# Optimization experiments

Hardware: AMD Instinct MI355X
Metric: run time of the kernel (lower is better)

Reference implementation:

```python
import jax, jax.numpy as jnp
import numpy as np

H = 1024
NUM_HEADS = 16
HEAD_DIM = H // NUM_HEADS
EPS = 1e-6
GEN_E, GEN_IE = 8, 4096 // 8     # general experts, per-expert intermediate
MOD_E, MOD_IE = 4, 4096 // 4     # per-modality experts, per-expert intermediate


def layernorm(x, g, b):
    m = jnp.mean(x, axis=-1, keepdims=True)
    v = jnp.mean((x - m) ** 2, axis=-1, keepdims=True)
    return (x - m) * jax.lax.rsqrt(v + EPS) * g + b


def attention(x, qkv_w, qkv_b, proj_w, proj_b):
    B, N, _ = x.shape
    qkv = (x @ qkv_w + qkv_b).reshape(B, N, 3, NUM_HEADS, HEAD_DIM)
    qkv = jnp.transpose(qkv, (2, 0, 3, 1, 4))  # [3,B,h,N,d]
    q, k, v = qkv[0], qkv[1], qkv[2]
    scale = HEAD_DIM ** -0.5
    attn = jax.nn.softmax(jnp.einsum('bhnd,bhmd->bhnm', q, k) * scale, axis=-1)
    out = jnp.einsum('bhnm,bhmd->bhnd', attn, v)
    out = jnp.transpose(out, (0, 2, 1, 3)).reshape(B, N, H)
    return out @ proj_w + proj_b


def routed_mlp(x, position_ids, gate_up, down, ie):
    # expert_id = position % num_experts; compute all experts then select per token
    # (avoids materializing per-token [T,H,2I] gathered weights).
    E = gate_up.shape[0]
    eids = position_ids % E  # [B,N]
    gu = jnp.einsum('bnh,ehi->bnei', x, gate_up)              # [B,N,E,2*ie]
    gu = jnp.take_along_axis(gu, eids[..., None, None], axis=2)[:, :, 0]
    gate, up = gu[..., :ie], gu[..., ie:]
    inter = jax.nn.silu(gate) * up                             # [B,N,ie]
    dn = jnp.einsum('bni,eih->bneh', inter, down)              # [B,N,E,H]
    return jnp.take_along_axis(dn, eids[..., None, None], axis=2)[:, :, 0]


def setup_inputs() -> dict:
    key = jax.random.key(0)
    ks = jax.random.split(key, 16)
    B, N = 2, 2048
    inp = {
        'x': jax.random.normal(ks[0], (B, N, H), jnp.float32),
        'qkv_w': jax.random.normal(ks[1], (H, 3 * H), jnp.float32) * 0.02,
        'qkv_b': jnp.zeros((3 * H,), jnp.float32),
        'proj_w': jax.random.normal(ks[2], (H, H), jnp.float32) * 0.02,
        'proj_b': jnp.zeros((H,), jnp.float32),
        'ln1_g': jnp.ones((H,), jnp.float32), 'ln1_b': jnp.zeros((H,), jnp.float32),
        'ln2_g': jnp.ones((H,), jnp.float32), 'ln2_b': jnp.zeros((H,), jnp.float32),
        'ln3_g': jnp.ones((H,), jnp.float32), 'ln3_b': jnp.zeros((H,), jnp.float32),
        'gen_gu': jax.random.normal(ks[3], (GEN_E, H, 2 * GEN_IE), jnp.float32) * 0.02,
        'gen_dn': jax.random.normal(ks[4], (GEN_E, GEN_IE, H), jnp.float32) * 0.02,
        'text_gu': jax.random.normal(ks[5], (MOD_E, H, 2 * MOD_IE), jnp.float32) * 0.02,
        'text_dn': jax.random.normal(ks[6], (MOD_E, MOD_IE, H), jnp.float32) * 0.02,
        'img_gu': jax.random.normal(ks[7], (MOD_E, H, 2 * MOD_IE), jnp.float32) * 0.02,
        'img_dn': jax.random.normal(ks[8], (MOD_E, MOD_IE, H), jnp.float32) * 0.02,
        'aud_gu': jax.random.normal(ks[9], (MOD_E, H, 2 * MOD_IE), jnp.float32) * 0.02,
        'aud_dn': jax.random.normal(ks[10], (MOD_E, MOD_IE, H), jnp.float32) * 0.02,
        'vid_gu': jax.random.normal(ks[11], (MOD_E, H, 2 * MOD_IE), jnp.float32) * 0.02,
        'vid_dn': jax.random.normal(ks[12], (MOD_E, MOD_IE, H), jnp.float32) * 0.02,
        'modality_ids': jax.random.randint(ks[13], (B, N), 0, 4, jnp.int32),
        'position_ids': jnp.arange(B * N, dtype=jnp.int32).reshape(B, N),
    }
    return inp


def reference(x, qkv_w, qkv_b, proj_w, proj_b,
              ln1_g, ln1_b, ln2_g, ln2_b, ln3_g, ln3_b,
              gen_gu, gen_dn, text_gu, text_dn, img_gu, img_dn,
              aud_gu, aud_dn, vid_gu, vid_dn,
              modality_ids, position_ids):
    x = x + attention(layernorm(x, ln1_g, ln1_b), qkv_w, qkv_b, proj_w, proj_b)
    x = x + routed_mlp(layernorm(x, ln2_g, ln2_b), position_ids, gen_gu, gen_dn, GEN_IE)
    normed = layernorm(x, ln3_g, ln3_b)
    tm = (modality_ids == 0)[..., None].astype(x.dtype)
    im = (modality_ids == 1)[..., None].astype(x.dtype)
    am = (modality_ids == 2)[..., None].astype(x.dtype)
    vm = (modality_ids == 3)[..., None].astype(x.dtype)
    x = x + (routed_mlp(normed, position_ids, text_gu, text_dn, MOD_IE) * tm
             + routed_mlp(normed, position_ids, img_gu, img_dn, MOD_IE) * im
             + routed_mlp(normed, position_ids, aud_gu, aud_dn, MOD_IE) * am
             + routed_mlp(normed, position_ids, vid_gu, vid_dn, MOD_IE) * vm)
    return x
```

## Files before the change

### kernel.cpp

```cpp
#include <hip/hip_runtime.h>

#define T_TOKENS 4096
#define HDIM 1024

typedef __attribute__((ext_vector_type(8))) short bf16x8;
typedef __attribute__((ext_vector_type(4))) float f32x4;

static __device__ inline unsigned short f2bf(float f) {
  unsigned u = __float_as_uint(f);
  unsigned r = (u + 0x7FFFu + ((u >> 16) & 1u)) >> 16;
  return (unsigned short)r;
}
static __device__ inline float bf2f(unsigned short h) {
  unsigned u = ((unsigned)h) << 16;
  return __uint_as_float(u);
}
static __device__ __forceinline__ void gl16(const void* g, void* l) {
  __builtin_amdgcn_global_load_lds((const __attribute__((address_space(1))) void*)g,
                                   (__attribute__((address_space(3))) void*)l, 16, 0, 0);
}

__launch_bounds__(256)
__global__ void ln_kernel(const float* __restrict__ in, const float* __restrict__ g,
                          const float* __restrict__ b, unsigned short* __restrict__ out) {
  const int row = blockIdx.x;
  const int tid = threadIdx.x;
  const long base = (long)row * HDIM;
  float4 v = *(const float4*)(in + base + tid * 4);
  __shared__ float red[256];
  red[tid] = v.x + v.y + v.z + v.w;
  __syncthreads();
  for (int st = 128; st > 0; st >>= 1) {
    if (tid < st) red[tid] += red[tid + st];
    __syncthreads();
  }
  const float mean = red[0] * (1.f / HDIM);
  __syncthreads();
  const float dx = v.x - mean, dy = v.y - mean, dz = v.z - mean, dw = v.w - mean;
  red[tid] = dx * dx + dy * dy + dz * dz + dw * dw;
  __syncthreads();
  for (int st = 128; st > 0; st >>= 1) {
    if (tid < st) red[tid] += red[tid + st];
    __syncthreads();
  }
  const float rstd = rsqrtf(red[0] * (1.f / HDIM) + 1e-6f);
  const int c = tid * 4;
  const float4 g4 = *(const float4*)(g + c);
  const float4 b4 = *(const float4*)(b + c);
  uint2 o;
  o.x = (unsigned)f2bf(dx * rstd * g4.x + b4.x) | ((unsigned)f2bf(dy * rstd * g4.y + b4.y) << 16);
  o.y = (unsigned)f2bf(dz * rstd * g4.z + b4.z) | ((unsigned)f2bf(dw * rstd * g4.w + b4.w) << 16);
  *(uint2*)(out + base + c) = o;
}

__launch_bounds__(256)
__global__ void build_groups(const int* __restrict__ pids, const int* __restrict__ mids,
                             int* __restrict__ gen_cnt, int* __restrict__ gen_list,
                             int* __restrict__ mod_cnt, int* __restrict__ mod_list) {
  const int t = blockIdx.x * 256 + threadIdx.x;
  if (t >= T_TOKENS) return;
  const int p = pids[t];
  const int ge = p & 7;
  int s = atomicAdd(&gen_cnt[ge], 1);
  if (s < 512) gen_list[ge * 512 + s] = t;
  const int g = mids[t] * 4 + (p & 3);
  s = atomicAdd(&mod_cnt[g], 1);
  if (s < 1024) mod_list[g * 1024 + s] = t;
}

__launch_bounds__(256)
__global__ void convert_w(const float* __restrict__ W, unsigned short* __restrict__ Wt,
                          int K, int N) {
  const long zo = (long)blockIdx.z * K * N;
  const float* Wp = W + zo;
  unsigned short* Wo = Wt + zo;
  const int n0 = blockIdx.x * 64, k0 = blockIdx.y * 64;
  __shared__ float T[64][65];
  const int tid = threadIdx.x;
#pragma unroll
  for (int i = 0; i < 4; ++i) {
    const int item = tid + i * 256;
    const int kk = item >> 4, c4 = (item & 15) * 4;
    const float4 v = *(const float4*)(Wp + (long)(k0 + kk) * N + n0 + c4);
    T[c4 + 0][kk] = v.x; T[c4 + 1][kk] = v.y; T[c4 + 2][kk] = v.z; T[c4 + 3][kk] = v.w;
  }
  __syncthreads();
#pragma unroll
  for (int i = 0; i < 4; ++i) {
    const int item = tid + i * 256;
    const int nn = item >> 4, k4 = (item & 15) * 4;
    uint2 p;
    p.x = (unsigned)f2bf(T[nn][k4 + 0]) | ((unsigned)f2bf(T[nn][k4 + 1]) << 16);
    p.y = (unsigned)f2bf(T[nn][k4 + 2]) | ((unsigned)f2bf(T[nn][k4 + 3]) << 16);
    *(uint2*)(Wo + (long)(n0 + nn) * K + k0 + k4) = p;
  }
}

enum { MODE_DENSE = 0, MODE_GEN = 1, MODE_MOD = 2 };
enum { OM_F32R = 0, OM_BF16 = 1, OM_QKV = 2 };

template <int MODE, int OMODE, bool WBF16, bool BIAS>
__launch_bounds__(256)
__global__ void mgemm(const unsigned short* __restrict__ A,
                      const void* __restrict__ w0, const float* __restrict__ w1,
                      const float* __restrict__ w2, const float* __restrict__ w3,
                      long wstep, const float* __restrict__ bias,
                      const float* __restrict__ resid, void* __restrict__ Cout,
                      unsigned short* __restrict__ qb, unsigned short* __restrict__ kb,
                      unsigned short* __restrict__ vtb,
                      int K, int N,
                      const int* __restrict__ cnts, const int* __restrict__ rowlist,
                      int cap) {
  const int z = blockIdx.z;
  const int n0 = blockIdx.x * 128;
  const int m0 = blockIdx.y * 128;

  int Meff = 1 << 30;
  const int* list = nullptr;
  if constexpr (MODE != MODE_DENSE) {
    Meff = cnts[z];
    if (m0 >= Meff) return;
    list = rowlist + z * cap;
  }

  __shared__ char As[128 * 64 * 2];
  __shared__ char Bs[128 * 64 * 2];

  const int tid = threadIdx.x;
  const int w = tid >> 6;
  const int lane = tid & 63;
  const int wm = w >> 1, wn = w & 1;
  const int srow = lane >> 3, sc = lane & 7;

  const unsigned short* asrc[4];
  char* aldsb = As + w * 4096;
#pragma unroll
  for (int i = 0; i < 4; ++i) {
    const int r = w * 32 + i * 8 + srow;
    long tok;
    if constexpr (MODE == MODE_DENSE) {
      tok = m0 + r;
    } else {
      int gm = m0 + r;
      if (gm >= Meff) gm = Meff - 1;
      tok = (long)list[gm];
    }
    asrc[i] = A + tok * (long)K + (sc ^ (r & 7)) * 8;
  }

  const unsigned short* bsrc[4];
  char* bldsb = Bs + w * 4096;
  const float* bptr[4];
  int boff[4];
  if constexpr (WBF16) {
    const unsigned short* W = (const unsigned short*)w0;
    if constexpr (MODE != MODE_DENSE) W += (long)z * wstep;
#pragma unroll
    for (int i = 0; i < 4; ++i) {
      const int r = w * 32 + i * 8 + srow;
      bsrc[i] = W + (long)(n0 + r) * K + (sc ^ (r & 7)) * 8;
    }
  } else {
    const float* W;
    if constexpr (MODE == MODE_MOD) {
      const int mm = z >> 2;
      const float* basep = (mm == 0) ? (const float*)w0 : (mm == 1) ? w1 : (mm == 2) ? w2 : w3;
      W = basep + (long)(z & 3) * wstep;
    } else {
      W = (const float*)w0 + (MODE != MODE_DENSE ? (long)z * wstep : 0);
    }
#pragma unroll
    for (int j = 0; j < 4; ++j) {
      const int item = tid + j * 256;
      const int kc = item >> 7;
      const int nl = item & 127;
      bptr[j] = W + (long)(kc * 8) * N + n0 + nl;
      boff[j] = (nl * 128 + kc * 16) ^ ((nl & 7) << 4);
    }
  }

  f32x4 acc[4][4] = {};

  for (int kt = 0; kt < K; kt += 64) {
    __syncthreads();
#pragma unroll
    for (int i = 0; i < 4; ++i) gl16(asrc[i] + kt, aldsb + i * 1024);
    if constexpr (WBF16) {
#pragma unroll
      for (int i = 0; i < 4; ++i) gl16(bsrc[i] + kt, bldsb + i * 1024);
    } else {
#pragma unroll
      for (int j = 0; j < 4; ++j) {
        const float* bp = bptr[j] + (long)kt * N;
        float kv[8];
#pragma unroll
        for (int u = 0; u < 8; ++u) kv[u] = bp[(long)u * N];
        uint4 p;
        p.x = (unsigned)f2bf(kv[0]) | ((unsigned)f2bf(kv[1]) << 16);
        p.y = (unsigned)f2bf(kv[2]) | ((unsigned)f2bf(kv[3]) << 16);
        p.z = (unsigned)f2bf(kv[4]) | ((unsigned)f2bf(kv[5]) << 16);
        p.w = (unsigned)f2bf(kv[6]) | ((unsigned)f2bf(kv[7]) << 16);
        *(uint4*)(Bs + boff[j]) = p;
      }
    }
    __syncthreads();

#pragma unroll
    for (int kk = 0; kk < 2; ++kk) {
      const int kb2 = kk * 64 + (lane >> 4) * 16;
      bf16x8 af[4], bfr[4];
#pragma unroll
      for (int f = 0; f < 4; ++f) {
        const int ar = wm * 64 + f * 16 + (lane & 15);
        af[f] = *(bf16x8*)(As + ((ar * 128 + kb2) ^ ((ar & 7) << 4)));
        const int br = wn * 64 + f * 16 + (lane & 15);
        bfr[f] = *(bf16x8*)(Bs + ((br * 128 + kb2) ^ ((br & 7) << 4)));
      }
#pragma unroll
      for (int mf = 0; mf < 4; ++mf)
#pragma unroll
        for (int nf = 0; nf < 4; ++nf)
          acc[mf][nf] =
              __builtin_amdgcn_mfma_f32_16x16x32_bf16(af[mf], bfr[nf], acc[mf][nf], 0, 0, 0);
    }
  }

  const int lr4 = (lane >> 4) * 4;
  const int lc = lane & 15;
#pragma unroll
  for (int mf = 0; mf < 4; ++mf) {
#pragma unroll
    for (int r = 0; r < 4; ++r) {
      const int gm = m0 + wm * 64 + mf * 16 + lr4 + r;
      long orow;
      if constexpr (MODE == MODE_DENSE) {
        orow = gm;
      } else {
        if (gm >= Meff) continue;
        orow = (long)list[gm];
      }
#pragma unroll
      for (int nf = 0; nf < 4; ++nf) {
        const int gc = n0 + wn * 64 + nf * 16 + lc;
        float val = acc[mf][nf][r];
        if constexpr (BIAS) val += bias[gc];
        if constexpr (OMODE == OM_F32R) {
          val += resid[orow * (long)N + gc];
          ((float*)Cout)[orow * (long)N + gc] = val;
        } else if constexpr (OMODE == OM_BF16) {
          ((unsigned short*)Cout)[orow * (long)N + gc] = f2bf(val);
        } else {
          const int bb = (int)(orow >> 11), tl = (int)orow & 2047;
          const int seg = gc >> 10, hc = gc & 1023, h = hc >> 6, d = hc & 63;
          if (seg == 0)
            qb[(((long)(bb * 16 + h) * 2048) + tl) * 64 + d] = f2bf(val * 0.125f);
          else if (seg == 1)
            kb[(((long)(bb * 16 + h) * 2048) + tl) * 64 + d] = f2bf(val);
          else
            vtb[((long)(bb * 16 + h) * 64 + d) * 2048 + tl] = f2bf(val);
        }
      }
    }
  }
}

__launch_bounds__(256)
__global__ void attn_kernel(const unsigned short* __restrict__ Qb,
                            const unsigned short* __restrict__ Kb,
                            const unsigned short* __restrict__ Vtb,
                            unsigned short* __restrict__ out) {
  const int qt = blockIdx.x;
  const int bh = blockIdx.y;
  const int b = bh >> 4, h = bh & 15;
  const int tid = threadIdx.x;
  const int w = tid >> 6;
  const int lane = tid & 63;
  const int srow = lane >> 3, sc = lane & 7;

  __shared__ char Ksb[8192];
  __shared__ char Vsb[8192];
  __shared__ char Psb[8192];
  char* Pwb = Psb + w * 2048;

  const unsigned short* Qh = Qb + ((long)(b * 16 + h) * 2048 + qt * 64) * 64;
  const unsigned short* Kh = Kb + (long)(b * 16 + h) * 2048 * 64;
  const unsigned short* Vh = Vtb + (long)(b * 16 + h) * 64 * 2048;

  bf16x8 qf[2];
  {
    const int qr = w * 16 + (lane & 15);
#pragma unroll
    for (int kst = 0; kst < 2; ++kst)
      qf[kst] = *(const bf16x8*)(Qh + qr * 64 + kst * 32 + (lane >> 4) * 8);
  }

  const unsigned short* ksrc[2];
  const unsigned short* vsrc[2];
  char* kld = Ksb + w * 2048;
  char* vld = Vsb + w * 2048;
#pragma unroll
  for (int i = 0; i < 2; ++i) {
    const int r = w * 16 + i * 8 + srow;
    ksrc[i] = Kh + (long)r * 64 + (sc ^ (r & 7)) * 8;
    vsrc[i] = Vh + (long)r * 2048 + (sc ^ (r & 7)) * 8;
  }

  float m_run[4] = {-1e30f, -1e30f, -1e30f, -1e30f};
  float l_run[4] = {0.f, 0.f, 0.f, 0.f};
  f32x4 acc[4] = {};

  for (int kt = 0; kt < 32; ++kt) {
    __syncthreads();
#pragma unroll
    for (int i = 0; i < 2; ++i) gl16(ksrc[i] + (long)kt * 64 * 64, kld + i * 1024);
#pragma unroll
    for (int i = 0; i < 2; ++i) gl16(vsrc[i] + kt * 64, vld + i * 1024);
    __syncthreads();

    f32x4 sf[4] = {};
    {
      const int cb = (lane >> 4) * 16;
#pragma unroll
      for (int f = 0; f < 4; ++f) {
        const int krow = f * 16 + (lane & 15);
        const int sw = (krow & 7) << 4;
        const bf16x8 k0 = *(bf16x8*)(Ksb + ((krow * 128 + cb) ^ sw));
        const bf16x8 k1 = *(bf16x8*)(Ksb + ((krow * 128 + 64 + cb) ^ sw));
        sf[f] = __builtin_amdgcn_mfma_f32_16x16x32_bf16(qf[0], k0, sf[f], 0, 0, 0);
        sf[f] = __builtin_amdgcn_mfma_f32_16x16x32_bf16(qf[1], k1, sf[f], 0, 0, 0);
      }
    }
    float al[4];
#pragma unroll
    for (int r = 0; r < 4; ++r) {
      float m0 = fmaxf(fmaxf(sf[0][r], sf[1][r]), fmaxf(sf[2][r], sf[3][r]));
      m0 = fmaxf(m0, __shfl_xor(m0, 1));
      m0 = fmaxf(m0, __shfl_xor(m0, 2));
      m0 = fmaxf(m0, __shfl_xor(m0, 4));
      m0 = fmaxf(m0, __shfl_xor(m0, 8));
      const float mn = fmaxf(m_run[r], m0);
      al[r] = __expf(m_run[r] - mn);
      m_run[r] = mn;
    }
#pragma unroll
    for (int f = 0; f < 4; ++f)
#pragma unroll
      for (int r = 0; r < 4; ++r) sf[f][r] = __expf(sf[f][r] - m_run[r]);
#pragma unroll
    for (int r = 0; r < 4; ++r) {
      float rs = sf[0][r] + sf[1][r] + sf[2][r] + sf[3][r];
      rs += __shfl_xor(rs, 1);
      rs += __shfl_xor(rs, 2);
      rs += __shfl_xor(rs, 4);
      rs += __shfl_xor(rs, 8);
      l_run[r] = l_run[r] * al[r] + rs;
    }
#pragma unroll
    for (int d = 0; d < 4; ++d)
#pragma unroll
      for (int r = 0; r < 4; ++r) acc[d][r] *= al[r];

#pragma unroll
    for (int f = 0; f < 4; ++f)
#pragma unroll
      for (int r = 0; r < 4; ++r) {
        const int prow = (lane >> 4) * 4 + r;
        const int off = (prow * 128 + (f * 16 + (lane & 15)) * 2) ^ ((prow & 7) << 4);
        *(short*)(Pwb + off) = (short)f2bf(sf[f][r]);
      }
    {
      const int cb = (lane >> 4) * 16;
      const int prow = lane & 15;
      const int psw = (prow & 7) << 4;
      const bf16x8 p0 = *(bf16x8*)(Pwb + ((prow * 128 + cb) ^ psw));
      const bf16x8 p1 = *(bf16x8*)(Pwb + ((prow * 128 + 64 + cb) ^ psw));
#pragma unroll
      for (int d = 0; d < 4; ++d) {
        const int vrow = d * 16 + (lane & 15);
        const int vsw = (vrow & 7) << 4;
        const bf16x8 v0 = *(bf16x8*)(Vsb + ((vrow * 128 + cb) ^ vsw));
        const bf16x8 v1 = *(bf16x8*)(Vsb + ((vrow * 128 + 64 + cb) ^ vsw));
        acc[d] = __builtin_amdgcn_mfma_f32_16x16x32_bf16(p0, v0, acc[d], 0, 0, 0);
        acc[d] = __builtin_amdgcn_mfma_f32_16x16x32_bf16(p1, v1, acc[d], 0, 0, 0);
      }
    }
  }

  float invl[4];
#pragma unroll
  for (int r = 0; r < 4; ++r) invl[r] = 1.f / l_run[r];
  unsigned short* op = out + (long)(b * 2048 + qt * 64 + w * 16) * 1024 + h * 64;
#pragma unroll
  for (int f = 0; f < 4; ++f)
#pragma unroll
    for (int r = 0; r < 4; ++r) {
      const int row = (lane >> 4) * 4 + r;
      op[(long)row * 1024 + f * 16 + (lane & 15)] = f2bf(acc[f][r] * invl[r]);
    }
}

__launch_bounds__(256)
__global__ void silu_bf(const unsigned short* __restrict__ gu, unsigned short* __restrict__ inter,
                        int IE2, int IE, int shift) {
  const int total = T_TOKENS << shift;
  for (int idx = blockIdx.x * 256 + threadIdx.x; idx < total; idx += gridDim.x * 256) {
    const int t = idx >> shift;
    const int r8 = (idx & ((1 << shift) - 1)) * 8;
    const unsigned short* gp = gu + (long)t * IE2 + r8;
    const uint4 gg = *(const uint4*)gp;
    const uint4 uu = *(const uint4*)(gp + IE);
    const unsigned gw[4] = {gg.x, gg.y, gg.z, gg.w};
    const unsigned uw[4] = {uu.x, uu.y, uu.z, uu.w};
    uint4 o;
    unsigned ow[4];
#pragma unroll
    for (int q = 0; q < 4; ++q) {
      const float g0 = __uint_as_float(gw[q] << 16);
      const float g1 = __uint_as_float(gw[q] & 0xffff0000u);
      const float u0 = __uint_as_float(uw[q] << 16);
      const float u1 = __uint_as_float(uw[q] & 0xffff0000u);
      const float r0 = g0 / (1.f + __expf(-g0)) * u0;
      const float r1 = g1 / (1.f + __expf(-g1)) * u1;
      ow[q] = (unsigned)f2bf(r0) | ((unsigned)f2bf(r1) << 16);
    }
    o.x = ow[0]; o.y = ow[1]; o.z = ow[2]; o.w = ow[3];
    *(uint4*)(inter + (long)t * IE + r8) = o;
  }
}

extern "C" void kernel_launch(void* const* d_in, const int* in_sizes, int n_in,
                              void* d_out, int out_size, void* d_ws, size_t ws_size,
                              hipStream_t stream) {
  const float* x       = (const float*)d_in[0];
  const float* qkv_w   = (const float*)d_in[1];
  const float* qkv_b   = (const float*)d_in[2];
  const float* proj_w  = (const float*)d_in[3];
  const float* proj_b  = (const float*)d_in[4];
  const float* ln1_g   = (const float*)d_in[5];
  const float* ln1_b   = (const float*)d_in[6];
  const float* ln2_g   = (const float*)d_in[7];
  const float* ln2_b   = (const float*)d_in[8];
  const float* ln3_g   = (const float*)d_in[9];
  const float* ln3_b   = (const float*)d_in[10];
  const float* gen_gu  = (const float*)d_in[11];
  const float* gen_dn  = (const float*)d_in[12];
  const float* text_gu = (const float*)d_in[13];
  const float* text_dn = (const float*)d_in[14];
  const float* img_gu  = (const float*)d_in[15];
  const float* img_dn  = (const float*)d_in[16];
  const float* aud_gu  = (const float*)d_in[17];
  const float* aud_dn  = (const float*)d_in[18];
  const float* vid_gu  = (const float*)d_in[19];
  const float* vid_dn  = (const float*)d_in[20];
  const int* mids      = (const int*)d_in[21];
  const int* pids      = (const int*)d_in[22];
  float* out = (float*)d_out;
  char* ws = (char*)d_ws;

  const unsigned long MB = 1ul << 20;
  unsigned short* lnb   = (unsigned short*)(ws);
  unsigned short* Qb    = (unsigned short*)(ws + 8 * MB);
  unsigned short* Kb    = (unsigned short*)(ws + 16 * MB);
  unsigned short* Vtb   = (unsigned short*)(ws + 24 * MB);
  unsigned short* attno = (unsigned short*)(ws + 32 * MB);
  unsigned short* wqkv  = (unsigned short*)(ws + 40 * MB);
  unsigned short* wproj = (unsigned short*)(ws + 46 * MB);
  unsigned short* wggu  = (unsigned short*)(ws + 48 * MB);
  unsigned short* wgdn  = (unsigned short*)(ws + 64 * MB);
  int* gen_cnt  = (int*)(ws + 72 * MB);
  int* mod_cnt  = gen_cnt + 8;
  int* gen_list = gen_cnt + 32;
  int* mod_list = gen_list + 8 * 512;
  unsigned short* guo    = Qb;
  unsigned short* intero = Vtb;

  hipMemsetAsync(gen_cnt, 0, (8 + 16) * sizeof(int), stream);
  build_groups<<<16, 256, 0, stream>>>(pids, mids, gen_cnt, gen_list, mod_cnt, mod_list);

  convert_w<<<dim3(48, 16, 1), 256, 0, stream>>>(qkv_w, wqkv, 1024, 3072);
  convert_w<<<dim3(16, 16, 1), 256, 0, stream>>>(proj_w, wproj, 1024, 1024);
  convert_w<<<dim3(16, 16, 8), 256, 0, stream>>>(gen_gu, wggu, 1024, 1024);
  convert_w<<<dim3(16, 8, 8), 256, 0, stream>>>(gen_dn, wgdn, 512, 1024);

  ln_kernel<<<4096, 256, 0, stream>>>(x, ln1_g, ln1_b, lnb);
  mgemm<MODE_DENSE, OM_QKV, true, true><<<dim3(24, 32, 1), 256, 0, stream>>>(
      lnb, wqkv, nullptr, nullptr, nullptr, 0L, qkv_b, nullptr, nullptr,
      Qb, Kb, Vtb, 1024, 3072, nullptr, nullptr, 0);
  attn_kernel<<<dim3(32, 32, 1), 256, 0, stream>>>(Qb, Kb, Vtb, attno);
  mgemm<MODE_DENSE, OM_F32R, true, true><<<dim3(8, 32, 1), 256, 0, stream>>>(
      attno, wproj, nullptr, nullptr, nullptr, 0L, proj_b, x, out,
      nullptr, nullptr, nullptr, 1024, 1024, nullptr, nullptr, 0);

  ln_kernel<<<4096, 256, 0, stream>>>(out, ln2_g, ln2_b, lnb);
  mgemm<MODE_GEN, OM_BF16, true, false><<<dim3(8, 4, 8), 256, 0, stream>>>(
      lnb, wggu, nullptr, nullptr, nullptr, (long)1024 * 1024, nullptr, nullptr, guo,
      nullptr, nullptr, nullptr, 1024, 1024, gen_cnt, gen_list, 512);
  silu_bf<<<1024, 256, 0, stream>>>(guo, intero, 1024, 512, 6);
  mgemm<MODE_GEN, OM_F32R, true, false><<<dim3(8, 4, 8), 256, 0, stream>>>(
      intero, wgdn, nullptr, nullptr, nullptr, (long)1024 * 512, nullptr, out, out,
      nullptr, nullptr, nullptr, 512, 1024, gen_cnt, gen_list, 512);

  ln_kernel<<<4096, 256, 0, stream>>>(out, ln3_g, ln3_b, lnb);
  mgemm<MODE_MOD, OM_BF16, false, false><<<dim3(16, 8, 16), 256, 0, stream>>>(
      lnb, text_gu, img_gu, aud_gu, vid_gu, (long)1024 * 2048, nullptr, nullptr, guo,
      nullptr, nullptr, nullptr, 1024, 2048, mod_cnt, mod_list, 1024);
  silu_bf<<<2048, 256, 0, stream>>>(guo, intero, 2048, 1024, 7);
  mgemm<MODE_MOD, OM_F32R, false, false><<<dim3(8, 8, 16), 256, 0, stream>>>(
      intero, text_dn, img_dn, aud_dn, vid_dn, (long)1024 * 1024, nullptr, out, out,
      nullptr, nullptr, nullptr, 1024, 1024, mod_cnt, mod_list, 1024);
}
```

Before: 460.2 us.

## Restructure attention to 128-key tiles with transposed scores and exp2 softmax

The attention kernel now processes 128 keys per iteration instead of 64 and computes S^T (K as the A operand), so each lane holds one query's scores and row max/sum need only two cross-lane shuffles. The log2(e) factor is folded into the Q scaling so exp2 can replace expf, and P is written to LDS packed as pairs. Separately, the manual bf16 rounding is replaced with the hardware v_cvt_pk_bf16_f32 instruction across the layernorm, weight-conversion, GEMM and SiLU kernels. The larger tile doubles LDS use per block, which can lower occupancy.

```diff
diff --git a/kernel.cpp b/kernel.cpp
--- a/kernel.cpp
+++ b/kernel.cpp
@@ -5,15 +5,18 @@
 
 typedef __attribute__((ext_vector_type(8))) short bf16x8;
 typedef __attribute__((ext_vector_type(4))) float f32x4;
+
+#define EXP2F(x) __builtin_amdgcn_exp2f(x)
 
 static __device__ inline unsigned short f2bf(float f) {
   unsigned u = __float_as_uint(f);
   unsigned r = (u + 0x7FFFu + ((u >> 16) & 1u)) >> 16;
   return (unsigned short)r;
 }
-static __device__ inline float bf2f(unsigned short h) {
-  unsigned u = ((unsigned)h) << 16;
-  return __uint_as_float(u);
+static __device__ __forceinline__ unsigned cvtpk(float lo, float hi) {
+  unsigned r;
+  asm("v_cvt_pk_bf16_f32 %0, %1, %2" : "=v"(r) : "v"(lo), "v"(hi));
+  return r;
 }
 static __device__ __forceinline__ void gl16(const void* g, void* l) {
   __builtin_amdgcn_global_load_lds((const __attribute__((address_space(1))) void*)g,
@@ -48,8 +51,8 @@
   const float4 g4 = *(const float4*)(g + c);
   const float4 b4 = *(const float4*)(b + c);
   uint2 o;
-  o.x = (unsigned)f2bf(dx * rstd * g4.x + b4.x) | ((unsigned)f2bf(dy * rstd * g4.y + b4.y) << 16);
-  o.y = (unsigned)f2bf(dz * rstd * g4.z + b4.z) | ((unsigned)f2bf(dw * rstd * g4.w + b4.w) << 16);
+  o.x = cvtpk(dx * rstd * g4.x + b4.x, dy * rstd * g4.y + b4.y);
+  o.y = cvtpk(dz * rstd * g4.z + b4.z, dw * rstd * g4.w + b4.w);
   *(uint2*)(out + base + c) = o;
 }
 
@@ -90,8 +93,8 @@
     const int item = tid + i * 256;
     const int nn = item >> 4, k4 = (item & 15) * 4;
     uint2 p;
-    p.x = (unsigned)f2bf(T[nn][k4 + 0]) | ((unsigned)f2bf(T[nn][k4 + 1]) << 16);
-    p.y = (unsigned)f2bf(T[nn][k4 + 2]) | ((unsigned)f2bf(T[nn][k4 + 3]) << 16);
+    p.x = cvtpk(T[nn][k4 + 0], T[nn][k4 + 1]);
+    p.y = cvtpk(T[nn][k4 + 2], T[nn][k4 + 3]);
     *(uint2*)(Wo + (long)(n0 + nn) * K + k0 + k4) = p;
   }
 }
@@ -196,10 +199,10 @@
 #pragma unroll
         for (int u = 0; u < 8; ++u) kv[u] = bp[(long)u * N];
         uint4 p;
-        p.x = (unsigned)f2bf(kv[0]) | ((unsigned)f2bf(kv[1]) << 16);
-        p.y = (unsigned)f2bf(kv[2]) | ((unsigned)f2bf(kv[3]) << 16);
-        p.z = (unsigned)f2bf(kv[4]) | ((unsigned)f2bf(kv[5]) << 16);
-        p.w = (unsigned)f2bf(kv[6]) | ((unsigned)f2bf(kv[7]) << 16);
+        p.x = cvtpk(kv[0], kv[1]);
+        p.y = cvtpk(kv[2], kv[3]);
+        p.z = cvtpk(kv[4], kv[5]);
+        p.w = cvtpk(kv[6], kv[7]);
         *(uint4*)(Bs + boff[j]) = p;
       }
     }
@@ -253,7 +256,7 @@
           const int bb = (int)(orow >> 11), tl = (int)orow & 2047;
           const int seg = gc >> 10, hc = gc & 1023, h = hc >> 6, d = hc & 63;
           if (seg == 0)
-            qb[(((long)(bb * 16 + h) * 2048) + tl) * 64 + d] = f2bf(val * 0.125f);
+            qb[(((long)(bb * 16 + h) * 2048) + tl) * 64 + d] = f2bf(val * 0.18033688011112042f);
           else if (seg == 1)
             kb[(((long)(bb * 16 + h) * 2048) + tl) * 64 + d] = f2bf(val);
           else
@@ -275,127 +278,121 @@
   const int tid = threadIdx.x;
   const int w = tid >> 6;
   const int lane = tid & 63;
-  const int srow = lane >> 3, sc = lane & 7;
-
-  __shared__ char Ksb[8192];
-  __shared__ char Vsb[8192];
-  __shared__ char Psb[8192];
-  char* Pwb = Psb + w * 2048;
+  const int g = lane >> 4;
+  const int q = lane & 15;
+
+  __shared__ char Ksb[128 * 128];
+  __shared__ char Vsb[64 * 256];
+  __shared__ char Psb[4 * 16 * 256];
+  char* Pwb = Psb + w * 4096;
 
   const unsigned short* Qh = Qb + ((long)(b * 16 + h) * 2048 + qt * 64) * 64;
   const unsigned short* Kh = Kb + (long)(b * 16 + h) * 2048 * 64;
   const unsigned short* Vh = Vtb + (long)(b * 16 + h) * 64 * 2048;
 
   bf16x8 qf[2];
-  {
-    const int qr = w * 16 + (lane & 15);
-#pragma unroll
-    for (int kst = 0; kst < 2; ++kst)
-      qf[kst] = *(const bf16x8*)(Qh + qr * 64 + kst * 32 + (lane >> 4) * 8);
-  }
-
-  const unsigned short* ksrc[2];
-  const unsigned short* vsrc[2];
-  char* kld = Ksb + w * 2048;
-  char* vld = Vsb + w * 2048;
-#pragma unroll
-  for (int i = 0; i < 2; ++i) {
-    const int r = w * 16 + i * 8 + srow;
-    ksrc[i] = Kh + (long)r * 64 + (sc ^ (r & 7)) * 8;
-    vsrc[i] = Vh + (long)r * 2048 + (sc ^ (r & 7)) * 8;
-  }
-
-  float m_run[4] = {-1e30f, -1e30f, -1e30f, -1e30f};
-  float l_run[4] = {0.f, 0.f, 0.f, 0.f};
+#pragma unroll
+  for (int kst = 0; kst < 2; ++kst)
+    qf[kst] = *(const bf16x8*)(Qh + (w * 16 + q) * 64 + kst * 32 + g * 8);
+
+  const unsigned short* ksrc[4];
+  const unsigned short* vsrc[4];
+  char* kld = Ksb + w * 4096;
+  char* vld = Vsb + w * 4096;
+#pragma unroll
+  for (int i = 0; i < 4; ++i) {
+    const int r = w * 32 + i * 8 + (lane >> 3);
+    ksrc[i] = Kh + (long)r * 64 + ((lane & 7) ^ (r & 7)) * 8;
+    const int d = w * 16 + i * 4 + (lane >> 4);
+    vsrc[i] = Vh + (long)d * 2048 + ((lane & 15) ^ (d & 7)) * 8;
+  }
+
+  float m_run = -1e30f, l_run = 0.f;
   f32x4 acc[4] = {};
-
-  for (int kt = 0; kt < 32; ++kt) {
+  const int qsw = (q & 7) << 4;
+
+  for (int kt = 0; kt < 16; ++kt) {
     __syncthreads();
 #pragma unroll
-    for (int i = 0; i < 2; ++i) gl16(ksrc[i] + (long)kt * 64 * 64, kld + i * 1024);
-#pragma unroll
-    for (int i = 0; i < 2; ++i) gl16(vsrc[i] + kt * 64, vld + i * 1024);
+    for (int i = 0; i < 4; ++i) gl16(ksrc[i] + (long)kt * 128 * 64, kld + i * 1024);
+#pragma unroll
+    for (int i = 0; i < 4; ++i) gl16(vsrc[i] + kt * 128, vld + i * 1024);
     __syncthreads();
 
-    f32x4 sf[4] = {};
-    {
-      const int cb = (lane >> 4) * 16;
-#pragma unroll
-      for (int f = 0; f < 4; ++f) {
-        const int krow = f * 16 + (lane & 15);
-        const int sw = (krow & 7) << 4;
-        const bf16x8 k0 = *(bf16x8*)(Ksb + ((krow * 128 + cb) ^ sw));
-        const bf16x8 k1 = *(bf16x8*)(Ksb + ((krow * 128 + 64 + cb) ^ sw));
-        sf[f] = __builtin_amdgcn_mfma_f32_16x16x32_bf16(qf[0], k0, sf[f], 0, 0, 0);
-        sf[f] = __builtin_amdgcn_mfma_f32_16x16x32_bf16(qf[1], k1, sf[f], 0, 0, 0);
+    f32x4 sf[8];
+#pragma unroll
+    for (int f = 0; f < 8; ++f) {
+      const int krow = f * 16 + q;
+      const int sw = (krow & 7) << 4;
+      const bf16x8 k0 = *(bf16x8*)(Ksb + krow * 128 + ((g * 16) ^ sw));
+      const bf16x8 k1 = *(bf16x8*)(Ksb + krow * 128 + ((64 + g * 16) ^ sw));
+      f32x4 t = {};
+      t = __builtin_amdgcn_mfma_f32_16x16x32_bf16(k0, qf[0], t, 0, 0, 0);
+      sf[f] = __builtin_amdgcn_mfma_f32_16x16x32_bf16(k1, qf[1], t, 0, 0, 0);
+    }
+
+    float mx = sf[0][0];
+#pragma unroll
+    for (int f = 0; f < 8; ++f) {
+      mx = fmaxf(mx, fmaxf(fmaxf(sf[f][0], sf[f][1]), fmaxf(sf[f][2], sf[f][3])));
+    }
+    mx = fmaxf(mx, __shfl_xor(mx, 16));
+    mx = fmaxf(mx, __shfl_xor(mx, 32));
+    const float mn = fmaxf(m_run, mx);
+    const float alpha = EXP2F(m_run - mn);
+    m_run = mn;
+
+    float ls = 0.f;
+#pragma unroll
+    for (int f = 0; f < 8; ++f) {
+#pragma unroll
+      for (int r = 0; r < 4; ++r) {
+        sf[f][r] = EXP2F(sf[f][r] - mn);
       }
-    }
-    float al[4];
+      ls += (sf[f][0] + sf[f][1]) + (sf[f][2] + sf[f][3]);
+    }
+    ls += __shfl_xor(ls, 16);
+    ls += __shfl_xor(ls, 32);
+    l_run = l_run * alpha + ls;
+
+#pragma unroll
+    for (int f = 0; f < 8; ++f) {
+      const unsigned p0 = cvtpk(sf[f][0], sf[f][1]);
+      const unsigned p1 = cvtpk(sf[f][2], sf[f][3]);
+      const int base = f * 32 + g * 8;
+      *(unsigned*)(Pwb + q * 256 + ((base) ^ qsw)) = p0;
+      *(unsigned*)(Pwb + q * 256 + ((base + 4) ^ qsw)) = p1;
+    }
+
 #pragma unroll
     for (int r = 0; r < 4; ++r) {
-      float m0 = fmaxf(fmaxf(sf[0][r], sf[1][r]), fmaxf(sf[2][r], sf[3][r]));
-      m0 = fmaxf(m0, __shfl_xor(m0, 1));
-      m0 = fmaxf(m0, __shfl_xor(m0, 2));
-      m0 = fmaxf(m0, __shfl_xor(m0, 4));
-      m0 = fmaxf(m0, __shfl_xor(m0, 8));
-      const float mn = fmaxf(m_run[r], m0);
-      al[r] = __expf(m_run[r] - mn);
-      m_run[r] = mn;
-    }
-#pragma unroll
-    for (int f = 0; f < 4; ++f)
-#pragma unroll
-      for (int r = 0; r < 4; ++r) sf[f][r] = __expf(sf[f][r] - m_run[r]);
+      const float aO = __shfl(alpha, g * 4 + r, 64);
+      acc[0][r] *= aO; acc[1][r] *= aO; acc[2][r] *= aO; acc[3][r] *= aO;
+    }
+
+#pragma unroll
+    for (int kst = 0; kst < 4; ++kst) {
+      const bf16x8 pa = *(bf16x8*)(Pwb + q * 256 + ((kst * 64 + g * 16) ^ qsw));
+#pragma unroll
+      for (int df = 0; df < 4; ++df) {
+        const int vrow = df * 16 + q;
+        const int vsw = (vrow & 7) << 4;
+        const bf16x8 vf = *(bf16x8*)(Vsb + vrow * 256 + ((kst * 64 + g * 16) ^ vsw));
+        acc[df] = __builtin_amdgcn_mfma_f32_16x16x32_bf16(pa, vf, acc[df], 0, 0, 0);
+      }
+    }
+  }
+
+  float linv[4];
+#pragma unroll
+  for (int r = 0; r < 4; ++r) linv[r] = 1.f / __shfl(l_run, g * 4 + r, 64);
+  unsigned short* op = out + (long)(b * 2048 + qt * 64 + w * 16) * 1024 + h * 64;
+#pragma unroll
+  for (int df = 0; df < 4; ++df)
 #pragma unroll
     for (int r = 0; r < 4; ++r) {
-      float rs = sf[0][r] + sf[1][r] + sf[2][r] + sf[3][r];
-      rs += __shfl_xor(rs, 1);
-      rs += __shfl_xor(rs, 2);
-      rs += __shfl_xor(rs, 4);
-      rs += __shfl_xor(rs, 8);
-      l_run[r] = l_run[r] * al[r] + rs;
-    }
-#pragma unroll
-    for (int d = 0; d < 4; ++d)
-#pragma unroll
-      for (int r = 0; r < 4; ++r) acc[d][r] *= al[r];
-
-#pragma unroll
-    for (int f = 0; f < 4; ++f)
-#pragma unroll
-      for (int r = 0; r < 4; ++r) {
-        const int prow = (lane >> 4) * 4 + r;
-        const int off = (prow * 128 + (f * 16 + (lane & 15)) * 2) ^ ((prow & 7) << 4);
-        *(short*)(Pwb + off) = (short)f2bf(sf[f][r]);
-      }
-    {
-      const int cb = (lane >> 4) * 16;
-      const int prow = lane & 15;
-      const int psw = (prow & 7) << 4;
-      const bf16x8 p0 = *(bf16x8*)(Pwb + ((prow * 128 + cb) ^ psw));
-      const bf16x8 p1 = *(bf16x8*)(Pwb + ((prow * 128 + 64 + cb) ^ psw));
-#pragma unroll
-      for (int d = 0; d < 4; ++d) {
-        const int vrow = d * 16 + (lane & 15);
-        const int vsw = (vrow & 7) << 4;
-        const bf16x8 v0 = *(bf16x8*)(Vsb + ((vrow * 128 + cb) ^ vsw));
-        const bf16x8 v1 = *(bf16x8*)(Vsb + ((vrow * 128 + 64 + cb) ^ vsw));
-        acc[d] = __builtin_amdgcn_mfma_f32_16x16x32_bf16(p0, v0, acc[d], 0, 0, 0);
-        acc[d] = __builtin_amdgcn_mfma_f32_16x16x32_bf16(p1, v1, acc[d], 0, 0, 0);
-      }
-    }
-  }
-
-  float invl[4];
-#pragma unroll
-  for (int r = 0; r < 4; ++r) invl[r] = 1.f / l_run[r];
-  unsigned short* op = out + (long)(b * 2048 + qt * 64 + w * 16) * 1024 + h * 64;
-#pragma unroll
-  for (int f = 0; f < 4; ++f)
-#pragma unroll
-    for (int r = 0; r < 4; ++r) {
-      const int row = (lane >> 4) * 4 + r;
-      op[(long)row * 1024 + f * 16 + (lane & 15)] = f2bf(acc[f][r] * invl[r]);
+      const int row = g * 4 + r;
+      op[(long)row * 1024 + df * 16 + q] = f2bf(acc[df][r] * linv[r]);
     }
 }
 
@@ -414,14 +411,14 @@
     uint4 o;
     unsigned ow[4];
 #pragma unroll
-    for (int q = 0; q < 4; ++q) {
-      const float g0 = __uint_as_float(gw[q] << 16);
-      const float g1 = __uint_as_float(gw[q] & 0xffff0000u);
-      const float u0 = __uint_as_float(uw[q] << 16);
-      const float u1 = __uint_as_float(uw[q] & 0xffff0000u);
+    for (int qq = 0; qq < 4; ++qq) {
+      const float g0 = __uint_as_float(gw[qq] << 16);
+      const float g1 = __uint_as_float(gw[qq] & 0xffff0000u);
+      const float u0 = __uint_as_float(uw[qq] << 16);
+      const float u1 = __uint_as_float(uw[qq] & 0xffff0000u);
       const float r0 = g0 / (1.f + __expf(-g0)) * u0;
       const float r1 = g1 / (1.f + __expf(-g1)) * u1;
-      ow[q] = (unsigned)f2bf(r0) | ((unsigned)f2bf(r1) << 16);
+      ow[qq] = cvtpk(r0, r1);
     }
     o.x = ow[0]; o.y = ow[1]; o.z = ow[2]; o.w = ow[3];
     *(uint4*)(inter + (long)t * IE + r8) = o;
@@ -474,7 +471,7 @@
   unsigned short* guo    = Qb;
   unsigned short* intero = Vtb;
 
-  hipMemsetAsync(gen_cnt, 0, (8 + 16) * sizeof(int), stream);
+  (void)hipMemsetAsync(gen_cnt, 0, (8 + 16) * sizeof(int), stream);
   build_groups<<<16, 256, 0, stream>>>(pids, mids, gen_cnt, gen_list, mod_cnt, mod_list);
 
   convert_w<<<dim3(48, 16, 1), 256, 0, stream>>>(qkv_w, wqkv, 1024, 3072);
```

Measured after the change: 417.3 us. -9.3%, faster.
